# Kernel tuning notes

Hardware: AMD Instinct MI355X
Metric: run time of the kernel (lower is better)

## Reference

```python
import jax, jax.numpy as jnp
import numpy as np

FIELD_DIMS = [26000] * 39
EMBED_DIM = 64
MLP_DIMS = [400, 400, 400]
BATCH = 16384
OFFSETS = jnp.asarray(np.concatenate(([0], np.cumsum(FIELD_DIMS)[:-1])), dtype=jnp.int32)
BN_INV = 1.0 / np.sqrt(1.0 + 1e-5)  # eval-mode BatchNorm1d: running_mean=0, running_var=1


def setup_inputs() -> dict:
    key = jax.random.key(0)
    ks = jax.random.split(key, 16)
    B, F, E = BATCH, len(FIELD_DIMS), EMBED_DIM
    V = sum(FIELD_DIMS)
    s = lambda k, shp, sc=0.05: (jax.random.normal(k, shp, jnp.float32) * sc)
    inp = {
        "x": jax.random.randint(ks[0], (B, F), 0, FIELD_DIMS[0], dtype=jnp.int32),
        "emb_table": s(ks[1], (V, E)),
        "lin_table": s(ks[2], (V, 1)),
        "lin_bias": jnp.zeros((1,), jnp.float32),
        "sparse_var": s(ks[3], (F, E), 0.1),
        "Wt": s(ks[4], (F, E, E)),  # per-field Linear weights, (out,in) layout
        "bt": jnp.zeros((F, E), jnp.float32),
    }
    dims = [F * E] + MLP_DIMS
    for i in range(3):
        inp[f"W{i+1}"] = s(ks[5 + i], (dims[i], dims[i + 1]))
        inp[f"b{i+1}"] = jnp.zeros((dims[i + 1],), jnp.float32)
        inp[f"g{i+1}"] = jnp.ones((dims[i + 1],), jnp.float32)
        inp[f"be{i+1}"] = jnp.zeros((dims[i + 1],), jnp.float32)
    inp["Wout"] = s(ks[9], (MLP_DIMS[-1], 1))
    inp["bout"] = jnp.zeros((1,), jnp.float32)
    return inp


def reference(x, emb_table, lin_table, lin_bias, sparse_var, Wt, bt,
              W1, b1, g1, be1, W2, b2, g2, be2, W3, b3, g3, be3, Wout, bout):
    B = x.shape[0]
    idx = x + OFFSETS[None, :]                       # (B, F) global vocab ids
    # sparse gate (detached in torch), eval-mode hard threshold mask
    sv = jax.nn.sigmoid(jax.lax.stop_gradient(sparse_var) * 15.0)
    sv = jnp.where(sv > 0.001, sv, 0.0)              # (F, E)
    embed_x = emb_table[idx] * sv                    # (B, F, E) gather + gate
    # per-field small Linear, batched as one einsum (torch: y = e @ W.T + b)
    trans = jnp.einsum('bfi,foi->bfo', embed_x, Wt) + bt  # (B, F, E)
    # FM second-order term
    sum_f = trans.sum(axis=1)                        # (B, E)
    fm = 0.5 * jnp.sum(sum_f * sum_f - (trans * trans).sum(axis=1),
                       axis=-1, keepdims=True)       # (B, 1)
    # first-order linear term
    lin = lin_table[idx].sum(axis=1) + lin_bias      # (B, 1)
    # MLP on flattened gated embeddings (Linear -> BN(eval) -> ReLU)
    h = embed_x.reshape(B, -1)
    for W, b, g, be in ((W1, b1, g1, be1), (W2, b2, g2, be2), (W3, b3, g3, be3)):
        h = jax.nn.relu((h @ W + b) * (BN_INV * g) + be)
    mlp = h @ Wout + bout                            # (B, 1)
    return jax.nn.sigmoid(jnp.squeeze(lin + fm + mlp, axis=1))  # (B,)
```

## Files before the change

kernel.cpp:

```cpp
#include <hip/hip_runtime.h>

#define BT 16384
#define NF 39
#define FD 26000

typedef unsigned short u16;
typedef unsigned int u32;
typedef short bf16x8 __attribute__((ext_vector_type(8)));
typedef float f32x4 __attribute__((ext_vector_type(4)));

__device__ __forceinline__ float bf2f(u16 h) {
  union { u32 u; float f; } v; v.u = ((u32)h) << 16; return v.f;
}
__device__ __forceinline__ u16 f2bf(float f) {
  union { float f; u32 u; } v; v.f = f;
  u32 r = v.u + 0x7fffu + ((v.u >> 16) & 1u);
  return (u16)(r >> 16);
}

__global__ __launch_bounds__(256) void k_embed(
    const int* __restrict__ x, const float* __restrict__ emb,
    const float* __restrict__ lin_table, const float* __restrict__ lin_bias,
    const float* __restrict__ sparse_var, const float* __restrict__ Wt,
    const float* __restrict__ bt, u16* __restrict__ h0, float* __restrict__ base)
{
  __shared__ u16                s_x[64 * NF];
  __shared__ float              s_sv[NF * 64];
  __shared__ float              s_bt[NF * 64];
  __shared__ __align__(16) u16  s_emb[64 * 72];
  __shared__ __align__(16) u16  s_wt[64 * 72];
  __shared__ float              s_S[64 * 65];
  __shared__ float              s_Q[64];

  const int tid = threadIdx.x;
  const int b0 = blockIdx.x * 64;

  for (int i = tid; i < 64 * NF; i += 256) s_x[i] = (u16)x[b0 * NF + i];
  for (int i = tid; i < NF * 64; i += 256) {
    float v = sparse_var[i];
    float s = 1.0f / (1.0f + __expf(-15.0f * v));
    s_sv[i] = (s > 0.001f) ? s : 0.0f;
    s_bt[i] = bt[i];
  }
  __syncthreads();

  const int wave = tid >> 6, lane = tid & 63;
  const int quad = lane >> 4, c16 = lane & 15;

  float q[4] = {0.f, 0.f, 0.f, 0.f};
  float accS[4][4];
  #pragma unroll
  for (int nt = 0; nt < 4; ++nt)
    #pragma unroll
    for (int r = 0; r < 4; ++r) accS[nt][r] = 0.f;

  for (int f = 0; f < NF; ++f) {
    #pragma unroll
    for (int it = 0; it < 4; ++it) {
      int s = tid + it * 256;
      int row = s >> 4, c4 = (s & 15) * 4;
      float4 w = *(const float4*)&Wt[f * 4096 + row * 64 + c4];
      union { uint2 v; u16 h[4]; } p;
      p.h[0] = f2bf(w.x); p.h[1] = f2bf(w.y);
      p.h[2] = f2bf(w.z); p.h[3] = f2bf(w.w);
      *(uint2*)&s_wt[row * 72 + c4] = p.v;
    }
    #pragma unroll
    for (int it = 0; it < 4; ++it) {
      int s = tid + it * 256;
      int row = s >> 4, c4 = (s & 15) * 4;
      long gi = (long)((int)s_x[row * NF + f] + f * FD);
      float4 e = *(const float4*)&emb[gi * 64 + c4];
      union { uint2 v; u16 h[4]; } p;
      p.h[0] = f2bf(e.x * s_sv[f * 64 + c4 + 0]);
      p.h[1] = f2bf(e.y * s_sv[f * 64 + c4 + 1]);
      p.h[2] = f2bf(e.z * s_sv[f * 64 + c4 + 2]);
      p.h[3] = f2bf(e.w * s_sv[f * 64 + c4 + 3]);
      *(uint2*)&s_emb[row * 72 + c4] = p.v;
      *(uint2*)&h0[(long)(b0 + row) * (NF * 64) + f * 64 + c4] = p.v;
    }
    __syncthreads();

    bf16x8 a0 = *(const bf16x8*)&s_emb[(wave * 16 + c16) * 72 + quad * 8];
    bf16x8 a1 = *(const bf16x8*)&s_emb[(wave * 16 + c16) * 72 + 32 + quad * 8];
    #pragma unroll
    for (int nt = 0; nt < 4; ++nt) {
      bf16x8 bb0 = *(const bf16x8*)&s_wt[(nt * 16 + c16) * 72 + quad * 8];
      bf16x8 bb1 = *(const bf16x8*)&s_wt[(nt * 16 + c16) * 72 + 32 + quad * 8];
      f32x4 acc = {0.f, 0.f, 0.f, 0.f};
      acc = __builtin_amdgcn_mfma_f32_16x16x32_bf16(a0, bb0, acc, 0, 0, 0);
      acc = __builtin_amdgcn_mfma_f32_16x16x32_bf16(a1, bb1, acc, 0, 0, 0);
      float btv = s_bt[f * 64 + nt * 16 + c16];
      #pragma unroll
      for (int r = 0; r < 4; ++r) {
        float t = acc[r] + btv;
        accS[nt][r] += t;
        q[r] += t * t;
      }
    }
    __syncthreads();
  }

  #pragma unroll
  for (int nt = 0; nt < 4; ++nt)
    #pragma unroll
    for (int r = 0; r < 4; ++r)
      s_S[(wave * 16 + quad * 4 + r) * 65 + nt * 16 + c16] = accS[nt][r];

  #pragma unroll
  for (int r = 0; r < 4; ++r) {
    float v = q[r];
    v += __shfl_xor(v, 1, 64);
    v += __shfl_xor(v, 2, 64);
    v += __shfl_xor(v, 4, 64);
    v += __shfl_xor(v, 8, 64);
    if (c16 == 0) s_Q[wave * 16 + quad * 4 + r] = v;
  }
  __syncthreads();

  if (tid < 64) {
    float s2 = 0.f;
    #pragma unroll 8
    for (int e = 0; e < 64; ++e) { float v = s_S[tid * 65 + e]; s2 += v * v; }
    float fmv = 0.5f * (s2 - s_Q[tid]);
    float lv = 0.f;
    #pragma unroll
    for (int f = 0; f < NF; ++f)
      lv += lin_table[(int)s_x[tid * NF + f] + f * FD];
    base[b0 + tid] = lv + lin_bias[0] + fmv;
  }
}

__global__ __launch_bounds__(256) void k_gemm(
    const u16* __restrict__ A, const u16* __restrict__ Bt, int K,
    const float* __restrict__ bias, const float* __restrict__ g,
    const float* __restrict__ be, u16* __restrict__ C)
{
  __shared__ __align__(16) u16 sA[128 * 40];
  __shared__ __align__(16) u16 sB[80 * 40];

  const int tid = threadIdx.x;
  int bid = blockIdx.x;
  int xcd = bid & 7;
  int j = bid >> 3;
  const int m0 = (xcd * 16 + j / 5) * 128;
  const int n0 = (j % 5) * 80;

  const int wave = tid >> 6, lane = tid & 63;
  const int quad = lane >> 4, c16 = lane & 15;

  f32x4 acc[2][5];
  #pragma unroll
  for (int mt = 0; mt < 2; ++mt)
    #pragma unroll
    for (int nt = 0; nt < 5; ++nt) acc[mt][nt] = {0.f, 0.f, 0.f, 0.f};

  for (int k0 = 0; k0 < K; k0 += 32) {
    #pragma unroll
    for (int it = 0; it < 2; ++it) {
      int s = tid + it * 256;
      int row = s >> 2, c = (s & 3) * 8;
      uint4 v = {0u, 0u, 0u, 0u};
      if (k0 + c < K) v = *(const uint4*)&A[(long)(m0 + row) * K + k0 + c];
      *(uint4*)&sA[row * 40 + c] = v;
    }
    for (int s = tid; s < 320; s += 256) {
      int row = s >> 2, c = (s & 3) * 8;
      uint4 v = {0u, 0u, 0u, 0u};
      if (k0 + c < K) v = *(const uint4*)&Bt[(long)(n0 + row) * K + k0 + c];
      *(uint4*)&sB[row * 40 + c] = v;
    }
    __syncthreads();

    bf16x8 a0 = *(const bf16x8*)&sA[(wave * 32 + c16) * 40 + quad * 8];
    bf16x8 a1 = *(const bf16x8*)&sA[(wave * 32 + 16 + c16) * 40 + quad * 8];
    #pragma unroll
    for (int nt = 0; nt < 5; ++nt) {
      bf16x8 b = *(const bf16x8*)&sB[(nt * 16 + c16) * 40 + quad * 8];
      acc[0][nt] = __builtin_amdgcn_mfma_f32_16x16x32_bf16(a0, b, acc[0][nt], 0, 0, 0);
      acc[1][nt] = __builtin_amdgcn_mfma_f32_16x16x32_bf16(a1, b, acc[1][nt], 0, 0, 0);
    }
    __syncthreads();
  }

  const float BN_INV = 0.9999950000374997f;
  #pragma unroll
  for (int nt = 0; nt < 5; ++nt) {
    int col = n0 + nt * 16 + c16;
    float bb = bias[col];
    float sc = BN_INV * g[col];
    float bv = be[col];
    #pragma unroll
    for (int mt = 0; mt < 2; ++mt) {
      #pragma unroll
      for (int r = 0; r < 4; ++r) {
        int row = m0 + wave * 32 + mt * 16 + quad * 4 + r;
        float y = (acc[mt][nt][r] + bb) * sc + bv;
        y = fmaxf(y, 0.f);
        C[(long)row * 400 + col] = f2bf(y);
      }
    }
  }
}

__global__ __launch_bounds__(256) void k_transpose(
    const float* __restrict__ in, u16* __restrict__ out, int R, int C)
{
  __shared__ u16 t[32][33];
  int c0 = blockIdx.x * 32, r0 = blockIdx.y * 32;
  int tx = threadIdx.x & 31, ty = threadIdx.x >> 5;
  for (int i = ty; i < 32; i += 8) {
    int r = r0 + i, c = c0 + tx;
    t[i][tx] = (r < R && c < C) ? f2bf(in[(long)r * C + c]) : (u16)0;
  }
  __syncthreads();
  for (int i = ty; i < 32; i += 8) {
    int c = c0 + i, r = r0 + tx;
    if (c < C && r < R) out[(long)c * R + r] = t[tx][i];
  }
}

__global__ __launch_bounds__(256) void k_final(
    const u16* __restrict__ h3, const float* __restrict__ Wout,
    const float* __restrict__ bout, const float* __restrict__ base,
    float* __restrict__ out)
{
  int wave = threadIdx.x >> 6, lane = threadIdx.x & 63;
  int b = blockIdx.x * 4 + wave;
  float s = 0.f;
  for (int jj = lane; jj < 400; jj += 64)
    s += bf2f(h3[(long)b * 400 + jj]) * Wout[jj];
  #pragma unroll
  for (int m = 32; m >= 1; m >>= 1) s += __shfl_xor(s, m, 64);
  if (lane == 0) {
    float z = s + base[b] + bout[0];
    out[b] = 1.0f / (1.0f + __expf(-z));
  }
}

extern "C" void kernel_launch(void* const* d_in, const int* in_sizes, int n_in,
                              void* d_out, int out_size, void* d_ws, size_t ws_size,
                              hipStream_t stream)
{
  const int*   x         = (const int*)d_in[0];
  const float* emb       = (const float*)d_in[1];
  const float* lin_table = (const float*)d_in[2];
  const float* lin_bias  = (const float*)d_in[3];
  const float* svar      = (const float*)d_in[4];
  const float* Wt        = (const float*)d_in[5];
  const float* bt        = (const float*)d_in[6];
  const float* W1  = (const float*)d_in[7];
  const float* b1  = (const float*)d_in[8];
  const float* g1  = (const float*)d_in[9];
  const float* be1 = (const float*)d_in[10];
  const float* W2  = (const float*)d_in[11];
  const float* b2  = (const float*)d_in[12];
  const float* g2  = (const float*)d_in[13];
  const float* be2 = (const float*)d_in[14];
  const float* W3  = (const float*)d_in[15];
  const float* b3  = (const float*)d_in[16];
  const float* g3  = (const float*)d_in[17];
  const float* be3 = (const float*)d_in[18];
  const float* Wo  = (const float*)d_in[19];
  const float* bo  = (const float*)d_in[20];

  char* ws = (char*)d_ws;
  size_t off = 0;
  u16* h0 = (u16*)(ws + off);   off += (size_t)BT * (NF * 64) * 2;
  u16* h1 = (u16*)(ws + off);   off += (size_t)BT * 400 * 2;
  u16* h2 = (u16*)(ws + off);   off += (size_t)BT * 400 * 2;
  float* base = (float*)(ws + off); off += (size_t)BT * 4;
  u16* W1T = (u16*)(ws + off);  off += (size_t)2496 * 400 * 2;
  u16* W2T = (u16*)(ws + off);  off += (size_t)400 * 400 * 2;
  u16* W3T = (u16*)(ws + off);  off += (size_t)400 * 400 * 2;
  (void)ws_size; (void)in_sizes; (void)n_in; (void)out_size;

  k_transpose<<<dim3(13, 78), 256, 0, stream>>>(W1, W1T, 2496, 400);
  k_transpose<<<dim3(13, 13), 256, 0, stream>>>(W2, W2T, 400, 400);
  k_transpose<<<dim3(13, 13), 256, 0, stream>>>(W3, W3T, 400, 400);
  k_embed<<<256, 256, 0, stream>>>(x, emb, lin_table, lin_bias, svar, Wt, bt,
                                   h0, base);
  k_gemm<<<640, 256, 0, stream>>>(h0, W1T, 2496, b1, g1, be1, h1);
  k_gemm<<<640, 256, 0, stream>>>(h1, W2T, 400, b2, g2, be2, h2);
  k_gemm<<<640, 256, 0, stream>>>(h2, W3T, 400, b3, g3, be3, h1);
  k_final<<<4096, 256, 0, stream>>>(h1, Wo, bo, base, (float*)d_out);
}
```

Measured before the change: 551.6 us.

## Use direct global-to-LDS loads with swizzled K=64 tiles, pad MLP buffers, retile embed

The GEMM now stages tiles with global_load_lds 16-byte transfers into XOR-swizzled 64-wide K tiles, so each barrier covers twice the K work and avoids register round-trips and bounds checks. This requires padding the hidden activations and transposed weights to 448 columns and zero-filling the pad. The embed kernel processes 32 rows per block with twice as many blocks, uses 16-byte loads and stores, and spreads the linear-term gather across all threads. The three weight transposes are merged into one launch. The padding adds extra memory and zero-writes, and correctness depends on the swizzle and LDS layout matching.

```diff
diff --git a/kernel.cpp b/kernel.cpp
--- a/kernel.cpp
+++ b/kernel.cpp
@@ -16,6 +16,12 @@
   union { float f; u32 u; } v; v.f = f;
   u32 r = v.u + 0x7fffu + ((v.u >> 16) & 1u);
   return (u16)(r >> 16);
+}
+
+__device__ __forceinline__ void gld16(const u16* g, u16* l) {
+  __builtin_amdgcn_global_load_lds(
+      (const __attribute__((address_space(1))) void*)g,
+      (__attribute__((address_space(3))) void*)l, 16, 0, 0);
 }
 
 __global__ __launch_bounds__(256) void k_embed(
@@ -24,18 +30,19 @@
     const float* __restrict__ sparse_var, const float* __restrict__ Wt,
     const float* __restrict__ bt, u16* __restrict__ h0, float* __restrict__ base)
 {
-  __shared__ u16                s_x[64 * NF];
+  __shared__ u16                s_x[32 * NF];
   __shared__ float              s_sv[NF * 64];
   __shared__ float              s_bt[NF * 64];
-  __shared__ __align__(16) u16  s_emb[64 * 72];
+  __shared__ __align__(16) u16  s_emb[32 * 72];
   __shared__ __align__(16) u16  s_wt[64 * 72];
-  __shared__ float              s_S[64 * 65];
-  __shared__ float              s_Q[64];
+  __shared__ float              s_S[32 * 65];
+  __shared__ float              s_Qp[64];
+  __shared__ float              s_lin[32];
 
   const int tid = threadIdx.x;
-  const int b0 = blockIdx.x * 64;
-
-  for (int i = tid; i < 64 * NF; i += 256) s_x[i] = (u16)x[b0 * NF + i];
+  const int b0 = blockIdx.x * 32;
+
+  for (int i = tid; i < 32 * NF; i += 256) s_x[i] = (u16)x[b0 * NF + i];
   for (int i = tid; i < NF * 64; i += 256) {
     float v = sparse_var[i];
     float s = 1.0f / (1.0f + __expf(-15.0f * v));
@@ -46,45 +53,51 @@
 
   const int wave = tid >> 6, lane = tid & 63;
   const int quad = lane >> 4, c16 = lane & 15;
+  const int mt = wave & 1, nh = wave >> 1;
 
   float q[4] = {0.f, 0.f, 0.f, 0.f};
-  float accS[4][4];
-  #pragma unroll
-  for (int nt = 0; nt < 4; ++nt)
-    #pragma unroll
-    for (int r = 0; r < 4; ++r) accS[nt][r] = 0.f;
+  float accS[2][4];
+  #pragma unroll
+  for (int j = 0; j < 2; ++j)
+    #pragma unroll
+    for (int r = 0; r < 4; ++r) accS[j][r] = 0.f;
+
+  const int g_row = tid >> 3, g_c8 = (tid & 7) * 8;
 
   for (int f = 0; f < NF; ++f) {
     #pragma unroll
-    for (int it = 0; it < 4; ++it) {
-      int s = tid + it * 256;
-      int row = s >> 4, c4 = (s & 15) * 4;
-      float4 w = *(const float4*)&Wt[f * 4096 + row * 64 + c4];
-      union { uint2 v; u16 h[4]; } p;
-      p.h[0] = f2bf(w.x); p.h[1] = f2bf(w.y);
-      p.h[2] = f2bf(w.z); p.h[3] = f2bf(w.w);
-      *(uint2*)&s_wt[row * 72 + c4] = p.v;
-    }
-    #pragma unroll
-    for (int it = 0; it < 4; ++it) {
-      int s = tid + it * 256;
-      int row = s >> 4, c4 = (s & 15) * 4;
-      long gi = (long)((int)s_x[row * NF + f] + f * FD);
-      float4 e = *(const float4*)&emb[gi * 64 + c4];
-      union { uint2 v; u16 h[4]; } p;
-      p.h[0] = f2bf(e.x * s_sv[f * 64 + c4 + 0]);
-      p.h[1] = f2bf(e.y * s_sv[f * 64 + c4 + 1]);
-      p.h[2] = f2bf(e.z * s_sv[f * 64 + c4 + 2]);
-      p.h[3] = f2bf(e.w * s_sv[f * 64 + c4 + 3]);
-      *(uint2*)&s_emb[row * 72 + c4] = p.v;
-      *(uint2*)&h0[(long)(b0 + row) * (NF * 64) + f * 64 + c4] = p.v;
+    for (int it = 0; it < 2; ++it) {
+      int row = g_row + it * 32;
+      float4 w0 = *(const float4*)&Wt[f * 4096 + row * 64 + g_c8];
+      float4 w1 = *(const float4*)&Wt[f * 4096 + row * 64 + g_c8 + 4];
+      union { uint4 v; u16 h[8]; } p;
+      p.h[0] = f2bf(w0.x); p.h[1] = f2bf(w0.y); p.h[2] = f2bf(w0.z); p.h[3] = f2bf(w0.w);
+      p.h[4] = f2bf(w1.x); p.h[5] = f2bf(w1.y); p.h[6] = f2bf(w1.z); p.h[7] = f2bf(w1.w);
+      *(uint4*)&s_wt[row * 72 + g_c8] = p.v;
+    }
+    {
+      long gi = (long)((int)s_x[g_row * NF + f] + f * FD);
+      float4 e0 = *(const float4*)&emb[gi * 64 + g_c8];
+      float4 e1 = *(const float4*)&emb[gi * 64 + g_c8 + 4];
+      union { uint4 v; u16 h[8]; } p;
+      p.h[0] = f2bf(e0.x * s_sv[f * 64 + g_c8 + 0]);
+      p.h[1] = f2bf(e0.y * s_sv[f * 64 + g_c8 + 1]);
+      p.h[2] = f2bf(e0.z * s_sv[f * 64 + g_c8 + 2]);
+      p.h[3] = f2bf(e0.w * s_sv[f * 64 + g_c8 + 3]);
+      p.h[4] = f2bf(e1.x * s_sv[f * 64 + g_c8 + 4]);
+      p.h[5] = f2bf(e1.y * s_sv[f * 64 + g_c8 + 5]);
+      p.h[6] = f2bf(e1.z * s_sv[f * 64 + g_c8 + 6]);
+      p.h[7] = f2bf(e1.w * s_sv[f * 64 + g_c8 + 7]);
+      *(uint4*)&s_emb[g_row * 72 + g_c8] = p.v;
+      *(uint4*)&h0[(long)(b0 + g_row) * 2496 + f * 64 + g_c8] = p.v;
     }
     __syncthreads();
 
-    bf16x8 a0 = *(const bf16x8*)&s_emb[(wave * 16 + c16) * 72 + quad * 8];
-    bf16x8 a1 = *(const bf16x8*)&s_emb[(wave * 16 + c16) * 72 + 32 + quad * 8];
-    #pragma unroll
-    for (int nt = 0; nt < 4; ++nt) {
+    bf16x8 a0 = *(const bf16x8*)&s_emb[(mt * 16 + c16) * 72 + quad * 8];
+    bf16x8 a1 = *(const bf16x8*)&s_emb[(mt * 16 + c16) * 72 + 32 + quad * 8];
+    #pragma unroll
+    for (int j = 0; j < 2; ++j) {
+      int nt = nh * 2 + j;
       bf16x8 bb0 = *(const bf16x8*)&s_wt[(nt * 16 + c16) * 72 + quad * 8];
       bf16x8 bb1 = *(const bf16x8*)&s_wt[(nt * 16 + c16) * 72 + 32 + quad * 8];
       f32x4 acc = {0.f, 0.f, 0.f, 0.f};
@@ -94,7 +107,7 @@
       #pragma unroll
       for (int r = 0; r < 4; ++r) {
         float t = acc[r] + btv;
-        accS[nt][r] += t;
+        accS[j][r] += t;
         q[r] += t * t;
       }
     }
@@ -102,10 +115,10 @@
   }
 
   #pragma unroll
-  for (int nt = 0; nt < 4; ++nt)
+  for (int j = 0; j < 2; ++j)
     #pragma unroll
     for (int r = 0; r < 4; ++r)
-      s_S[(wave * 16 + quad * 4 + r) * 65 + nt * 16 + c16] = accS[nt][r];
+      s_S[(mt * 16 + quad * 4 + r) * 65 + (nh * 2 + j) * 16 + c16] = accS[j][r];
 
   #pragma unroll
   for (int r = 0; r < 4; ++r) {
@@ -114,30 +127,37 @@
     v += __shfl_xor(v, 2, 64);
     v += __shfl_xor(v, 4, 64);
     v += __shfl_xor(v, 8, 64);
-    if (c16 == 0) s_Q[wave * 16 + quad * 4 + r] = v;
+    if (c16 == 0) s_Qp[nh * 32 + mt * 16 + quad * 4 + r] = v;
+  }
+
+  {
+    int row = tid >> 3, fi = tid & 7;
+    float lv = 0.f;
+    for (int f = fi; f < NF; f += 8)
+      lv += lin_table[(int)s_x[row * NF + f] + f * FD];
+    lv += __shfl_xor(lv, 1, 64);
+    lv += __shfl_xor(lv, 2, 64);
+    lv += __shfl_xor(lv, 4, 64);
+    if (fi == 0) s_lin[row] = lv;
   }
   __syncthreads();
 
-  if (tid < 64) {
+  if (tid < 32) {
     float s2 = 0.f;
     #pragma unroll 8
     for (int e = 0; e < 64; ++e) { float v = s_S[tid * 65 + e]; s2 += v * v; }
-    float fmv = 0.5f * (s2 - s_Q[tid]);
-    float lv = 0.f;
-    #pragma unroll
-    for (int f = 0; f < NF; ++f)
-      lv += lin_table[(int)s_x[tid * NF + f] + f * FD];
-    base[b0 + tid] = lv + lin_bias[0] + fmv;
+    float fmv = 0.5f * (s2 - (s_Qp[tid] + s_Qp[32 + tid]));
+    base[b0 + tid] = s_lin[tid] + lin_bias[0] + fmv;
   }
 }
 
 __global__ __launch_bounds__(256) void k_gemm(
-    const u16* __restrict__ A, const u16* __restrict__ Bt, int K,
-    const float* __restrict__ bias, const float* __restrict__ g,
-    const float* __restrict__ be, u16* __restrict__ C)
-{
-  __shared__ __align__(16) u16 sA[128 * 40];
-  __shared__ __align__(16) u16 sB[80 * 40];
+    const u16* __restrict__ A, int lda, const u16* __restrict__ Bt, int ldb,
+    int kit, const float* __restrict__ bias, const float* __restrict__ g,
+    const float* __restrict__ be, u16* __restrict__ C, int ldc)
+{
+  __shared__ __align__(16) u16 sA[128 * 64];
+  __shared__ __align__(16) u16 sB[80 * 64];
 
   const int tid = threadIdx.x;
   int bid = blockIdx.x;
@@ -149,36 +169,41 @@
   const int wave = tid >> 6, lane = tid & 63;
   const int quad = lane >> 4, c16 = lane & 15;
 
+  const int srow = lane >> 3;
+  const int sclog = (lane & 7) ^ (srow & 7);
+  const u16* gA = A + (long)m0 * lda + sclog * 8;
+  const u16* gB = Bt + (long)n0 * ldb + sclog * 8;
+
   f32x4 acc[2][5];
   #pragma unroll
-  for (int mt = 0; mt < 2; ++mt)
-    #pragma unroll
-    for (int nt = 0; nt < 5; ++nt) acc[mt][nt] = {0.f, 0.f, 0.f, 0.f};
-
-  for (int k0 = 0; k0 < K; k0 += 32) {
-    #pragma unroll
-    for (int it = 0; it < 2; ++it) {
-      int s = tid + it * 256;
-      int row = s >> 2, c = (s & 3) * 8;
-      uint4 v = {0u, 0u, 0u, 0u};
-      if (k0 + c < K) v = *(const uint4*)&A[(long)(m0 + row) * K + k0 + c];
-      *(uint4*)&sA[row * 40 + c] = v;
-    }
-    for (int s = tid; s < 320; s += 256) {
-      int row = s >> 2, c = (s & 3) * 8;
-      uint4 v = {0u, 0u, 0u, 0u};
-      if (k0 + c < K) v = *(const uint4*)&Bt[(long)(n0 + row) * K + k0 + c];
-      *(uint4*)&sB[row * 40 + c] = v;
-    }
+  for (int mtt = 0; mtt < 2; ++mtt)
+    #pragma unroll
+    for (int nt = 0; nt < 5; ++nt) acc[mtt][nt] = {0.f, 0.f, 0.f, 0.f};
+
+  for (int kk = 0; kk < kit; ++kk) {
+    const int k0 = kk * 64;
+    #pragma unroll
+    for (int it = 0; it < 4; ++it) {
+      int s = wave * 4 + it;
+      gld16(gA + (long)(s * 8 + srow) * lda + k0, &sA[s * 512]);
+    }
+    gld16(gB + (long)(wave * 8 + srow) * ldb + k0, &sB[wave * 512]);
+    gld16(gB + (long)((wave + 4) * 8 + srow) * ldb + k0, &sB[(wave + 4) * 512]);
+    if (wave < 2)
+      gld16(gB + (long)((wave + 8) * 8 + srow) * ldb + k0, &sB[(wave + 8) * 512]);
     __syncthreads();
 
-    bf16x8 a0 = *(const bf16x8*)&sA[(wave * 32 + c16) * 40 + quad * 8];
-    bf16x8 a1 = *(const bf16x8*)&sA[(wave * 32 + 16 + c16) * 40 + quad * 8];
-    #pragma unroll
-    for (int nt = 0; nt < 5; ++nt) {
-      bf16x8 b = *(const bf16x8*)&sB[(nt * 16 + c16) * 40 + quad * 8];
-      acc[0][nt] = __builtin_amdgcn_mfma_f32_16x16x32_bf16(a0, b, acc[0][nt], 0, 0, 0);
-      acc[1][nt] = __builtin_amdgcn_mfma_f32_16x16x32_bf16(a1, b, acc[1][nt], 0, 0, 0);
+    #pragma unroll
+    for (int ks = 0; ks < 2; ++ks) {
+      const int co = ((ks * 4 + quad) ^ (c16 & 7)) * 8;
+      bf16x8 a0 = *(const bf16x8*)&sA[(wave * 32 + c16) * 64 + co];
+      bf16x8 a1 = *(const bf16x8*)&sA[(wave * 32 + 16 + c16) * 64 + co];
+      #pragma unroll
+      for (int nt = 0; nt < 5; ++nt) {
+        bf16x8 b = *(const bf16x8*)&sB[(nt * 16 + c16) * 64 + co];
+        acc[0][nt] = __builtin_amdgcn_mfma_f32_16x16x32_bf16(a0, b, acc[0][nt], 0, 0, 0);
+        acc[1][nt] = __builtin_amdgcn_mfma_f32_16x16x32_bf16(a1, b, acc[1][nt], 0, 0, 0);
+      }
     }
     __syncthreads();
   }
@@ -191,23 +216,39 @@
     float sc = BN_INV * g[col];
     float bv = be[col];
     #pragma unroll
-    for (int mt = 0; mt < 2; ++mt) {
+    for (int mtt = 0; mtt < 2; ++mtt) {
       #pragma unroll
       for (int r = 0; r < 4; ++r) {
-        int row = m0 + wave * 32 + mt * 16 + quad * 4 + r;
-        float y = (acc[mt][nt][r] + bb) * sc + bv;
+        int row = m0 + wave * 32 + mtt * 16 + quad * 4 + r;
+        float y = (acc[mtt][nt][r] + bb) * sc + bv;
         y = fmaxf(y, 0.f);
-        C[(long)row * 400 + col] = f2bf(y);
+        C[(long)row * ldc + col] = f2bf(y);
       }
     }
   }
-}
-
-__global__ __launch_bounds__(256) void k_transpose(
-    const float* __restrict__ in, u16* __restrict__ out, int R, int C)
-{
+  if (ldc > 400 && n0 == 320) {
+    int npad = ldc - 400;
+    for (int s = tid; s < 128 * npad; s += 256) {
+      int rr = s / npad, cc = s % npad;
+      C[(long)(m0 + rr) * ldc + 400 + cc] = 0;
+    }
+  }
+}
+
+__global__ __launch_bounds__(256) void k_transpose3(
+    const float* __restrict__ W1, u16* __restrict__ W1T,
+    const float* __restrict__ W2, u16* __restrict__ W2T,
+    const float* __restrict__ W3, u16* __restrict__ W3T)
+{
+  int z = blockIdx.z;
+  const float* in = (z == 0) ? W1 : (z == 1) ? W2 : W3;
+  u16* out = (z == 0) ? W1T : (z == 1) ? W2T : W3T;
+  int R = (z == 0) ? 2496 : 400;
+  int Rpad = (z == 0) ? 2496 : 448;
+  const int C = 400;
+  int r0 = blockIdx.y * 32, c0 = blockIdx.x * 32;
+  if (r0 >= Rpad) return;
   __shared__ u16 t[32][33];
-  int c0 = blockIdx.x * 32, r0 = blockIdx.y * 32;
   int tx = threadIdx.x & 31, ty = threadIdx.x >> 5;
   for (int i = ty; i < 32; i += 8) {
     int r = r0 + i, c = c0 + tx;
@@ -216,7 +257,7 @@
   __syncthreads();
   for (int i = ty; i < 32; i += 8) {
     int c = c0 + i, r = r0 + tx;
-    if (c < C && r < R) out[(long)c * R + r] = t[tx][i];
+    if (c < C && r < Rpad) out[(long)c * Rpad + r] = t[tx][i];
   }
 }
 
@@ -229,7 +270,7 @@
   int b = blockIdx.x * 4 + wave;
   float s = 0.f;
   for (int jj = lane; jj < 400; jj += 64)
-    s += bf2f(h3[(long)b * 400 + jj]) * Wout[jj];
+    s += bf2f(h3[(long)b * 448 + jj]) * Wout[jj];
   #pragma unroll
   for (int m = 32; m >= 1; m >>= 1) s += __shfl_xor(s, m, 64);
   if (lane == 0) {
@@ -266,22 +307,21 @@
 
   char* ws = (char*)d_ws;
   size_t off = 0;
-  u16* h0 = (u16*)(ws + off);   off += (size_t)BT * (NF * 64) * 2;
-  u16* h1 = (u16*)(ws + off);   off += (size_t)BT * 400 * 2;
-  u16* h2 = (u16*)(ws + off);   off += (size_t)BT * 400 * 2;
+  u16* h0 = (u16*)(ws + off);   off += (size_t)BT * 2496 * 2;
+  u16* h1 = (u16*)(ws + off);   off += (size_t)BT * 448 * 2;
+  u16* h2 = (u16*)(ws + off);   off += (size_t)BT * 448 * 2;
+  u16* h3 = (u16*)(ws + off);   off += (size_t)BT * 448 * 2;
   float* base = (float*)(ws + off); off += (size_t)BT * 4;
-  u16* W1T = (u16*)(ws + off);  off += (size_t)2496 * 400 * 2;
-  u16* W2T = (u16*)(ws + off);  off += (size_t)400 * 400 * 2;
-  u16* W3T = (u16*)(ws + off);  off += (size_t)400 * 400 * 2;
+  u16* W1T = (u16*)(ws + off);  off += (size_t)400 * 2496 * 2;
+  u16* W2T = (u16*)(ws + off);  off += (size_t)400 * 448 * 2;
+  u16* W3T = (u16*)(ws + off);  off += (size_t)400 * 448 * 2;
   (void)ws_size; (void)in_sizes; (void)n_in; (void)out_size;
 
-  k_transpose<<<dim3(13, 78), 256, 0, stream>>>(W1, W1T, 2496, 400);
-  k_transpose<<<dim3(13, 13), 256, 0, stream>>>(W2, W2T, 400, 400);
-  k_transpose<<<dim3(13, 13), 256, 0, stream>>>(W3, W3T, 400, 400);
-  k_embed<<<256, 256, 0, stream>>>(x, emb, lin_table, lin_bias, svar, Wt, bt,
+  k_transpose3<<<dim3(13, 78, 3), 256, 0, stream>>>(W1, W1T, W2, W2T, W3, W3T);
+  k_embed<<<512, 256, 0, stream>>>(x, emb, lin_table, lin_bias, svar, Wt, bt,
                                    h0, base);
-  k_gemm<<<640, 256, 0, stream>>>(h0, W1T, 2496, b1, g1, be1, h1);
-  k_gemm<<<640, 256, 0, stream>>>(h1, W2T, 400, b2, g2, be2, h2);
-  k_gemm<<<640, 256, 0, stream>>>(h2, W3T, 400, b3, g3, be3, h1);
-  k_final<<<4096, 256, 0, stream>>>(h1, Wo, bo, base, (float*)d_out);
-}
+  k_gemm<<<640, 256, 0, stream>>>(h0, 2496, W1T, 2496, 39, b1, g1, be1, h1, 448);
+  k_gemm<<<640, 256, 0, stream>>>(h1, 448, W2T, 448, 7, b2, g2, be2, h2, 448);
+  k_gemm<<<640, 256, 0, stream>>>(h2, 448, W3T, 448, 7, b3, g3, be3, h3, 448);
+  k_final<<<4096, 256, 0, stream>>>(h3, Wo, bo, base, (float*)d_out);
+}
```

Result: faster. 480.0 us (-13.0%).
